# Kernel optimization log

Measured on AMD Instinct MI355X. Metric: run time of the kernel, lower is better.

Reference implementation:

```python
import jax, jax.numpy as jnp
import numpy as np

N = 200000   # nodes
E = 600000   # edges
D = 128      # emb_dim
L = 5        # num_layer
G = 2000     # graphs in batch
T = 1        # num_tasks
NUM_ATOM_TYPE = 120
NUM_CHIRALITY = 3
NUM_BOND_TYPE = 6
NUM_BOND_DIR = 3
EPS = 1e-5


def setup_inputs() -> dict:
    key = jax.random.key(0)
    ks = jax.random.split(key, 16)
    s = lambda k, shape, fan: jax.random.normal(k, shape, jnp.float32) * (1.0 / np.sqrt(fan))
    return {
        "x_idx": jax.random.randint(ks[0], (N, 2), 0, 3),
        "edge_index": jax.random.randint(ks[1], (2, E), 0, N),
        "edge_attr": jax.random.randint(ks[2], (E, 2), 0, 3),
        "batch": jnp.sort(jax.random.randint(ks[3], (N,), 0, G)),
        "atom_emb1": s(ks[4], (NUM_ATOM_TYPE, D), D),
        "atom_emb2": s(ks[5], (NUM_CHIRALITY, D), D),
        "edge_emb1": s(ks[6], (L, NUM_BOND_TYPE, D), D),
        "edge_emb2": s(ks[7], (L, NUM_BOND_DIR, D), D),
        "W1": s(ks[8], (L, D, 2 * D), D),
        "b1": jnp.zeros((L, 2 * D), jnp.float32),
        "W2": s(ks[9], (L, 2 * D, D), 2 * D),
        "b2": jnp.zeros((L, D), jnp.float32),
        "bn_gamma": jnp.ones((L, D), jnp.float32),
        "bn_beta": jnp.zeros((L, D), jnp.float32),
        "Wp": s(ks[10], (D, T), D),
        "bp": jnp.zeros((T,), jnp.float32),
    }


def reference(atom_emb1, atom_emb2, edge_emb1, edge_emb2, W1, b1, W2, b2,
              bn_gamma, bn_beta, Wp, bp, x_idx, edge_index, edge_attr, batch):
    # node input embedding: sum of atom-type and chirality embeddings
    h = atom_emb1[x_idx[:, 0]] + atom_emb2[x_idx[:, 1]]  # [N, D]
    src, dst = edge_index[0], edge_index[1]
    ea0, ea1 = edge_attr[:, 0], edge_attr[:, 1]
    for l in range(L):
        # GINConv: edge embedding + neighbor add-aggregation (incl. self loop, bond type 4 / dir 0)
        e = edge_emb1[l][ea0] + edge_emb2[l][ea1]                 # [E, D]
        msg = h[src] + e                                          # gather + fuse
        agg = jax.ops.segment_sum(msg, dst, num_segments=N)       # scatter-add
        agg = agg + h + (edge_emb1[l][4] + edge_emb2[l][0])       # self-loop message
        # GIN MLP: Linear(D,2D) -> ReLU -> Linear(2D,D)
        z = jnp.maximum(agg @ W1[l] + b1[l], 0.0) @ W2[l] + b2[l]
        # BatchNorm1d over nodes (training-mode batch statistics)
        mu = z.mean(0)
        var = z.var(0)
        z = (z - mu) * jax.lax.rsqrt(var + EPS) * bn_gamma[l] + bn_beta[l]
        # ReLU except after the last layer; dropout ratio is 0 (identity)
        h = jnp.maximum(z, 0.0) if l < L - 1 else z
    # JK 'last' node representation -> sum pooling over graphs -> task head
    pooled = jax.ops.segment_sum(h, batch, num_segments=G)        # [G, D]
    return pooled @ Wp + bp                                       # [G, T]
```

## Files before the change

### kernel.cpp

```cpp
#include <hip/hip_runtime.h>

typedef unsigned int uint;
typedef unsigned short ushort;
typedef _Float16 f16_t;
typedef f16_t f16x8 __attribute__((ext_vector_type(8)));
typedef ushort ushort8 __attribute__((ext_vector_type(8)));
typedef float f32x4 __attribute__((ext_vector_type(4)));

#define NN 200000
#define EE 600000
#define LL 5
#define GG 2000
#define SCAN_NB 782

__device__ __forceinline__ ushort f2h(float f) {
  f16_t h = (f16_t)f;
  return __builtin_bit_cast(ushort, h);
}
__device__ __forceinline__ float h2f(ushort u) {
  return (float)__builtin_bit_cast(f16_t, u);
}
__device__ __forceinline__ float hlo(uint u) { return h2f((ushort)(u & 0xFFFFu)); }
__device__ __forceinline__ float hhi(uint u) { return h2f((ushort)(u >> 16)); }
__device__ __forceinline__ f16x8 ld8h(const uint4* p, int idx) {
  uint4 u = p[idx];
  return __builtin_bit_cast(f16x8, u);
}
__device__ __forceinline__ f16x8 bnrelu8(f16x8 u, f16x8 sc, f16x8 sh) {
  f16x8 r = u * sc + sh;
#pragma unroll
  for (int j = 0; j < 8; ++j) r[j] = r[j] > (f16_t)0.f ? r[j] : (f16_t)0.f;
  return r;
}

__global__ void k_setup(const float* __restrict__ W1, const float* __restrict__ W2,
                        ushort* __restrict__ w1s, ushort* __restrict__ w2s,
                        const float* __restrict__ ee1, const float* __restrict__ ee2,
                        const float* __restrict__ at1, const float* __restrict__ at2,
                        ushort* __restrict__ tabh, const int* __restrict__ xidx,
                        int* __restrict__ xcode, float* __restrict__ out,
                        const float* __restrict__ bp) {
  int i = blockIdx.x * 256 + threadIdx.x;
  if (i < 40960) {
    int lane = i & 63;
    int f = i >> 6;
    bool isW2 = false;
    if (f >= 320) { f -= 320; isW2 = true; }
    int l = f >> 6, rem = f & 63;
    ushort8 o;
    if (!isW2) {
      int kt = rem >> 4, nt = rem & 15;
      int n = nt * 16 + (lane & 15);
      int kbase = kt * 32 + (lane >> 4) * 8;
#pragma unroll
      for (int j = 0; j < 8; ++j) o[j] = f2h(W1[l * 32768 + (kbase + j) * 256 + n]);
      *(ushort8*)(w1s + f * 512 + lane * 8) = o;
    } else {
      int kt = rem >> 3, nt = rem & 7;
      int n = nt * 16 + (lane & 15);
      int kbase = kt * 32 + (lane >> 4) * 8;
#pragma unroll
      for (int j = 0; j < 8; ++j) o[j] = f2h(W2[l * 32768 + (kbase + j) * 128 + n]);
      *(ushort8*)(w2s + f * 512 + lane * 8) = o;
    }
  }
  if (i < 5760) {
    int l = i / 1152, rem = i % 1152;
    int ab = rem >> 7, c = rem & 127;
    int a = ab / 3, b = ab - a * 3;
    tabh[i] = f2h(ee1[(l * 6 + a) * 128 + c] + ee2[(l * 3 + b) * 128 + c]);
  } else if (i < 6400) {
    int j = i - 5760;
    int l = j >> 7, c = j & 127;
    tabh[i] = f2h(ee1[(l * 6 + 4) * 128 + c] + ee2[(l * 3 + 0) * 128 + c]);
  } else if (i < 7552) {
    int j = i - 6400;
    int ab = j >> 7, c = j & 127;
    int a = ab / 3, b = ab - a * 3;
    tabh[i] = f2h(at1[a * 128 + c] + at2[b * 128 + c]);
  }
  if (i < NN) xcode[i] = xidx[2 * i] * 3 + xidx[2 * i + 1];
  if (i < GG) out[i] = bp[0];
}

__global__ void k_count(const int* __restrict__ ei, int* __restrict__ counts) {
  int e = blockIdx.x * 256 + threadIdx.x;
  if (e < EE) atomicAdd(&counts[ei[EE + e]], 1);
}

__global__ void k_scanA(const int* __restrict__ counts, int* __restrict__ rowptr,
                        int* __restrict__ bsums) {
  __shared__ int sd[256];
  int tid = threadIdx.x;
  int g = blockIdx.x * 256 + tid;
  int v = (g < NN) ? counts[g] : 0;
  sd[tid] = v;
  __syncthreads();
  for (int o = 1; o < 256; o <<= 1) {
    int t = (tid >= o) ? sd[tid - o] : 0;
    __syncthreads();
    sd[tid] += t;
    __syncthreads();
  }
  if (g < NN) rowptr[g] = sd[tid] - v;
  if (tid == 255) bsums[blockIdx.x] = sd[tid];
}

__global__ void k_scanB(int* __restrict__ bsums) {
  __shared__ int sd[1024];
  int tid = threadIdx.x;
  int v = (tid < SCAN_NB) ? bsums[tid] : 0;
  sd[tid] = v;
  __syncthreads();
  for (int o = 1; o < 1024; o <<= 1) {
    int t = (tid >= o) ? sd[tid - o] : 0;
    __syncthreads();
    sd[tid] += t;
    __syncthreads();
  }
  if (tid < SCAN_NB) bsums[tid] = sd[tid] - v;
}

__global__ void k_scanC(int* __restrict__ rowptr, const int* __restrict__ bsums) {
  int g = blockIdx.x * 256 + threadIdx.x;
  if (g < NN) rowptr[g] += bsums[blockIdx.x];
  if (g == 0) rowptr[NN] = EE;
}

__global__ void k_fill(const int* __restrict__ ei, const int* __restrict__ ea,
                       const int* __restrict__ xcode, int* __restrict__ cursor,
                       int* __restrict__ eslot) {
  int e = blockIdx.x * 256 + threadIdx.x;
  if (e < EE) {
    int dst = ei[EE + e];
    int src = ei[e];
    int a9 = ea[2 * e] * 3 + ea[2 * e + 1];
    int sc = xcode[src];
    int pos = atomicAdd(&cursor[dst], 1);
    eslot[pos] = src | (a9 << 18) | (sc << 22);
  }
}

__global__ void k_hist2(const int* __restrict__ rowptr, int* __restrict__ bhist) {
  __shared__ int h[256];
  int tid = threadIdx.x;
  h[tid] = 0;
  __syncthreads();
  int n = blockIdx.x * 256 + tid;
  if (n < NN) {
    int d = rowptr[n + 1] - rowptr[n];
    if (d > 255) d = 255;
    atomicAdd(&h[d], 1);
  }
  __syncthreads();
  bhist[tid * SCAN_NB + blockIdx.x] = h[tid];
}

__global__ void k_hscanA(int* __restrict__ data, int* __restrict__ bsums) {
  __shared__ int sd[256];
  int tid = threadIdx.x;
  int g = blockIdx.x * 256 + tid;
  int v = data[g];
  sd[tid] = v;
  __syncthreads();
  for (int o = 1; o < 256; o <<= 1) {
    int t = (tid >= o) ? sd[tid - o] : 0;
    __syncthreads();
    sd[tid] += t;
    __syncthreads();
  }
  data[g] = sd[tid] - v;
  if (tid == 255) bsums[blockIdx.x] = sd[tid];
}

__global__ void k_hscanC(int* __restrict__ data, const int* __restrict__ bsums) {
  int g = blockIdx.x * 256 + threadIdx.x;
  data[g] += bsums[blockIdx.x];
}

__global__ void k_dfill2(const int* __restrict__ rowptr, const int* __restrict__ xcode,
                         const int* __restrict__ bpos, int4* __restrict__ ndesc) {
  __shared__ int h[256];
  int tid = threadIdx.x;
  h[tid] = 0;
  __syncthreads();
  int n = blockIdx.x * 256 + tid;
  if (n < NN) {
    int s = rowptr[n], e = rowptr[n + 1];
    int d = e - s;
    if (d > 255) d = 255;
    int r = atomicAdd(&h[d], 1);
    int pos = bpos[d * SCAN_NB + blockIdx.x] + r;
    ndesc[pos] = make_int4(n, s, e, xcode[n]);
  }
}

__global__ __launch_bounds__(256, 5) void k_layer(
    const ushort* __restrict__ zin, ushort* __restrict__ zout,
    const int4* __restrict__ ndesc, const ushort* __restrict__ tabh,
    const float* __restrict__ bnscale, const float* __restrict__ bnshift,
    const int* __restrict__ eslot,
    const ushort* __restrict__ w1s, const ushort* __restrict__ w2s,
    const float* __restrict__ b1, const float* __restrict__ b2,
    float* __restrict__ stats, int layer) {
  __shared__ __align__(16) ushort BUF[32 * 264];
  __shared__ int4 ND[32];
  ushort* AGG = BUF;
  ushort* T1 = BUF;
  ushort* ldsZ = BUF;
  const int tid = threadIdx.x;
  const int w = tid >> 6, lane = tid & 63;
  const int ln16 = lane & 15, sub = lane >> 4;
  const int row0 = blockIdx.x * 32;

  if (tid < 32) ND[tid] = ndesc[row0 + tid];
  __syncthreads();

  const uint4* combH = (const uint4*)(tabh + (size_t)layer * 1152);
  const uint4* atomH = (const uint4*)(tabh + 6400);
  const uint4* selfH = (const uint4*)(tabh + 5760 + layer * 128);
  const uint4* h4 = (const uint4*)zin;
  f16x8 sf = ld8h(selfH, ln16);
  f16x8 scv = {}, shv = {};
  if (layer > 0) {
    const float* sp = bnscale + (layer - 1) * 128 + ln16 * 8;
    const float* hp = bnshift + (layer - 1) * 128 + ln16 * 8;
#pragma unroll
    for (int j = 0; j < 8; ++j) {
      scv[j] = (f16_t)sp[j];
      shv[j] = (f16_t)hp[j];
    }
  }

#pragma unroll
  for (int grp = 0; grp < 2; ++grp) {
    const int4 nd = ND[w * 8 + grp * 4 + sub];
    const int n = nd.x;
    const int s = nd.y, e = nd.z;
    f16x8 acc;
    if (layer == 0) {
      acc = ld8h(atomH, nd.w * 16 + ln16) + sf;
    } else {
      acc = bnrelu8(ld8h(h4, (size_t)n * 16 + ln16), scv, shv) + sf;
    }
    for (int base = s; base < e; base += 16) {
      int m = e - base;
      if (m > 16) m = 16;
      int slot = (ln16 < m) ? eslot[base + ln16] : 0;
      int jfull = m & ~3;
      int j = 0;
      for (; j < jfull; j += 4) {
        int sl0 = __shfl(slot, sub * 16 + j + 0, 64);
        int sl1 = __shfl(slot, sub * 16 + j + 1, 64);
        int sl2 = __shfl(slot, sub * 16 + j + 2, 64);
        int sl3 = __shfl(slot, sub * 16 + j + 3, 64);
        f16x8 p0, p1, p2, p3;
        if (layer == 0) {
          p0 = ld8h(atomH, ((sl0 >> 22) & 15) * 16 + ln16);
          p1 = ld8h(atomH, ((sl1 >> 22) & 15) * 16 + ln16);
          p2 = ld8h(atomH, ((sl2 >> 22) & 15) * 16 + ln16);
          p3 = ld8h(atomH, ((sl3 >> 22) & 15) * 16 + ln16);
        } else {
          p0 = ld8h(h4, (size_t)(sl0 & 0x3FFFF) * 16 + ln16);
          p1 = ld8h(h4, (size_t)(sl1 & 0x3FFFF) * 16 + ln16);
          p2 = ld8h(h4, (size_t)(sl2 & 0x3FFFF) * 16 + ln16);
          p3 = ld8h(h4, (size_t)(sl3 & 0x3FFFF) * 16 + ln16);
        }
        f16x8 c0 = ld8h(combH, ((sl0 >> 18) & 15) * 16 + ln16);
        f16x8 c1 = ld8h(combH, ((sl1 >> 18) & 15) * 16 + ln16);
        f16x8 c2 = ld8h(combH, ((sl2 >> 18) & 15) * 16 + ln16);
        f16x8 c3 = ld8h(combH, ((sl3 >> 18) & 15) * 16 + ln16);
        if (layer != 0) {
          p0 = bnrelu8(p0, scv, shv);
          p1 = bnrelu8(p1, scv, shv);
          p2 = bnrelu8(p2, scv, shv);
          p3 = bnrelu8(p3, scv, shv);
        }
        acc += p0 + c0;
        acc += p1 + c1;
        acc += p2 + c2;
        acc += p3 + c3;
      }
      for (; j < m; ++j) {
        int sl = __shfl(slot, sub * 16 + j, 64);
        f16x8 p0;
        if (layer == 0) {
          p0 = ld8h(atomH, ((sl >> 22) & 15) * 16 + ln16);
        } else {
          p0 = bnrelu8(ld8h(h4, (size_t)(sl & 0x3FFFF) * 16 + ln16), scv, shv);
        }
        f16x8 c0 = ld8h(combH, ((sl >> 18) & 15) * 16 + ln16);
        acc += p0 + c0;
      }
    }
    *(uint4*)&AGG[(w * 8 + grp * 4 + sub) * 136 + ln16 * 8] =
        __builtin_bit_cast(uint4, acc);
  }
  __syncthreads();

  const int lm = ln16, q = sub;
  f32x4 acc[2][4] = {};
  const ushort* w1b = w1s + layer * 64 * 512;
#pragma unroll
  for (int kt = 0; kt < 4; ++kt) {
    f16x8 af[2];
#pragma unroll
    for (int mt = 0; mt < 2; ++mt) {
      const ushort* p = AGG + (mt * 16 + lm) * 136 + kt * 32 + q * 8;
      af[mt] = __builtin_bit_cast(f16x8, *(const ushort8*)p);
    }
#pragma unroll
    for (int np = 0; np < 2; ++np) {
      f16x8 bf[2];
#pragma unroll
      for (int ni = 0; ni < 2; ++ni) {
        const ushort* p = w1b + (kt * 16 + w * 4 + np * 2 + ni) * 512 + lane * 8;
        bf[ni] = __builtin_bit_cast(f16x8, *(const ushort8*)p);
      }
#pragma unroll
      for (int mt = 0; mt < 2; ++mt)
#pragma unroll
        for (int ni = 0; ni < 2; ++ni)
          acc[mt][np * 2 + ni] = __builtin_amdgcn_mfma_f32_16x16x32_f16(
              af[mt], bf[ni], acc[mt][np * 2 + ni], 0, 0, 0);
    }
  }
  __syncthreads();
#pragma unroll
  for (int nt = 0; nt < 4; ++nt) {
    int n = w * 64 + nt * 16 + lm;
    float bias = b1[layer * 256 + n];
#pragma unroll
    for (int mt = 0; mt < 2; ++mt)
#pragma unroll
      for (int r = 0; r < 4; ++r) {
        float v = fmaxf(acc[mt][nt][r] + bias, 0.0f);
        T1[(mt * 16 + q * 4 + r) * 264 + n] = f2h(v);
      }
  }
  __syncthreads();

  f32x4 acc2[2][2] = {};
  const ushort* w2b = w2s + layer * 64 * 512;
#pragma unroll
  for (int kt = 0; kt < 8; ++kt) {
    f16x8 af[2], bf[2];
#pragma unroll
    for (int mt = 0; mt < 2; ++mt) {
      const ushort* p = T1 + (mt * 16 + lm) * 264 + kt * 32 + q * 8;
      af[mt] = __builtin_bit_cast(f16x8, *(const ushort8*)p);
    }
#pragma unroll
    for (int nt = 0; nt < 2; ++nt) {
      const ushort* p = w2b + (kt * 8 + w * 2 + nt) * 512 + lane * 8;
      bf[nt] = __builtin_bit_cast(f16x8, *(const ushort8*)p);
    }
#pragma unroll
    for (int mt = 0; mt < 2; ++mt)
#pragma unroll
      for (int nt = 0; nt < 2; ++nt)
        acc2[mt][nt] = __builtin_amdgcn_mfma_f32_16x16x32_f16(af[mt], bf[nt], acc2[mt][nt], 0, 0, 0);
  }
  __syncthreads();
  float ssum[2], ssq[2];
#pragma unroll
  for (int nt = 0; nt < 2; ++nt) {
    int n = w * 32 + nt * 16 + lm;
    float bias = b2[layer * 128 + n];
    ssum[nt] = 0.f;
    ssq[nt] = 0.f;
#pragma unroll
    for (int mt = 0; mt < 2; ++mt)
#pragma unroll
      for (int r = 0; r < 4; ++r) {
        float v = acc2[mt][nt][r] + bias;
        ldsZ[(mt * 16 + q * 4 + r) * 136 + n] = f2h(v);
        ssum[nt] += v;
        ssq[nt] += v * v;
      }
    ssum[nt] += __shfl_xor(ssum[nt], 16, 64);
    ssum[nt] += __shfl_xor(ssum[nt], 32, 64);
    ssq[nt] += __shfl_xor(ssq[nt], 16, 64);
    ssq[nt] += __shfl_xor(ssq[nt], 32, 64);
  }
  if (lane < 16) {
    int cp = blockIdx.x & 15;
    float* sb = stats + (size_t)(layer * 16 + cp) * 256;
#pragma unroll
    for (int nt = 0; nt < 2; ++nt) {
      int col = w * 32 + nt * 16 + lane;
      atomicAdd(&sb[col], ssum[nt]);
      atomicAdd(&sb[128 + col], ssq[nt]);
    }
  }
  __syncthreads();
  uint* zo = (uint*)zout;
  for (int i = tid; i < 32 * 64; i += 256) {
    int row = i >> 6, cpx = i & 63;
    uint v = *(const uint*)&ldsZ[row * 136 + cpx * 2];
    zo[(size_t)ND[row].x * 64 + cpx] = v;
  }
}

__global__ void k_bnparam(const float* __restrict__ stats, const float* __restrict__ gamma,
                          const float* __restrict__ beta, float* __restrict__ bnscale,
                          float* __restrict__ bnshift, int layer) {
  int c = threadIdx.x;
  float s = 0.f, qv = 0.f;
  for (int cp = 0; cp < 16; ++cp) {
    const float* sb = stats + (size_t)(layer * 16 + cp) * 256;
    s += sb[c];
    qv += sb[128 + c];
  }
  float mu = s * (1.0f / NN);
  float var = qv * (1.0f / NN) - mu * mu;
  float sc = gamma[layer * 128 + c] * rsqrtf(var + 1e-5f);
  bnscale[layer * 128 + c] = sc;
  bnshift[layer * 128 + c] = beta[layer * 128 + c] - mu * sc;
}

__global__ __launch_bounds__(256) void k_pool(const ushort* __restrict__ z,
                                              const float* __restrict__ bnscale,
                                              const float* __restrict__ bnshift,
                                              const int* __restrict__ batch,
                                              const float* __restrict__ Wp,
                                              float* __restrict__ out) {
  const int tid = threadIdx.x;
  const int w = tid >> 6, lane = tid & 63;
  const int nb = blockIdx.x * 64 + w * 16;
  float2 wp = ((const float2*)Wp)[lane];
  float2 scv = ((const float2*)(bnscale + 4 * 128))[lane];
  float2 shv = ((const float2*)(bnshift + 4 * 128))[lane];
  const uint* z32 = (const uint*)z;
  int bb = (lane < 16) ? batch[nb + lane] : 0;
  int curb = __shfl(bb, 0);
  float run = 0.f;
#pragma unroll
  for (int i = 0; i < 16; ++i) {
    int b = __shfl(bb, i);
    uint u = z32[(size_t)(nb + i) * 64 + lane];
    float dot = fmaf(hlo(u), scv.x, shv.x) * wp.x + fmaf(hhi(u), scv.y, shv.y) * wp.y;
#pragma unroll
    for (int off = 32; off > 0; off >>= 1) dot += __shfl_xor(dot, off, 64);
    if (b != curb) {
      if (lane == 0) atomicAdd(&out[curb], run);
      run = 0.f;
      curb = b;
    }
    run += dot;
  }
  if (lane == 0) atomicAdd(&out[curb], run);
}

extern "C" void kernel_launch(void* const* d_in, const int* in_sizes, int n_in,
                              void* d_out, int out_size, void* d_ws, size_t ws_size,
                              hipStream_t stream) {
  (void)in_sizes; (void)n_in; (void)out_size; (void)ws_size;
  const int* xidx = (const int*)d_in[0];
  const int* eidx = (const int*)d_in[1];
  const int* eattr = (const int*)d_in[2];
  const int* batch = (const int*)d_in[3];
  const float* at1 = (const float*)d_in[4];
  const float* at2 = (const float*)d_in[5];
  const float* ee1 = (const float*)d_in[6];
  const float* ee2 = (const float*)d_in[7];
  const float* W1 = (const float*)d_in[8];
  const float* b1 = (const float*)d_in[9];
  const float* W2 = (const float*)d_in[10];
  const float* b2 = (const float*)d_in[11];
  const float* gamma = (const float*)d_in[12];
  const float* beta = (const float*)d_in[13];
  const float* Wp = (const float*)d_in[14];
  const float* bp = (const float*)d_in[15];
  float* out = (float*)d_out;

  char* ws = (char*)d_ws;
  size_t off = 0;
  auto alloc = [&](size_t bytes) -> void* {
    void* p = ws + off;
    off = (off + bytes + 255) & ~(size_t)255;
    return p;
  };
  ushort* bufA = (ushort*)alloc((size_t)NN * 128 * 2);
  ushort* bufB = (ushort*)alloc((size_t)NN * 128 * 2);
  ushort* w1s = (ushort*)alloc(320 * 512 * 2);
  ushort* w2s = (ushort*)alloc(320 * 512 * 2);
  int* rowptr = (int*)alloc((NN + 1) * 4);
  int* cursor = (int*)alloc((size_t)NN * 4);
  int* eslot = (int*)alloc((size_t)EE * 4);
  int* bsums = (int*)alloc(1024 * 4);
  ushort* tabh = (ushort*)alloc(7552 * 2);
  int* xcode = (int*)alloc((size_t)NN * 4);
  float* stats = (float*)alloc((size_t)LL * 16 * 256 * 4);
  float* bnscale = (float*)alloc(LL * 128 * 4);
  float* bnshift = (float*)alloc(LL * 128 * 4);
  int* bhist = (int*)alloc((size_t)SCAN_NB * 256 * 4);
  int* bsums2 = (int*)alloc(1024 * 4);
  int4* ndesc = (int4*)alloc((size_t)NN * 16);

  hipMemsetAsync(cursor, 0, (size_t)NN * 4, stream);
  hipMemsetAsync(stats, 0, (size_t)LL * 16 * 256 * 4, stream);
  k_setup<<<SCAN_NB, 256, 0, stream>>>(W1, W2, w1s, w2s, ee1, ee2, at1, at2, tabh, xidx,
                                       xcode, out, bp);
  k_count<<<(EE + 255) / 256, 256, 0, stream>>>(eidx, cursor);
  k_scanA<<<SCAN_NB, 256, 0, stream>>>(cursor, rowptr, bsums);
  k_scanB<<<1, 1024, 0, stream>>>(bsums);
  k_scanC<<<SCAN_NB, 256, 0, stream>>>(rowptr, bsums);
  hipMemcpyAsync(cursor, rowptr, (size_t)NN * 4, hipMemcpyDeviceToDevice, stream);
  k_fill<<<(EE + 255) / 256, 256, 0, stream>>>(eidx, eattr, xcode, cursor, eslot);
  k_hist2<<<SCAN_NB, 256, 0, stream>>>(rowptr, bhist);
  k_hscanA<<<SCAN_NB, 256, 0, stream>>>(bhist, bsums2);
  k_scanB<<<1, 1024, 0, stream>>>(bsums2);
  k_hscanC<<<SCAN_NB, 256, 0, stream>>>(bhist, bsums2);
  k_dfill2<<<SCAN_NB, 256, 0, stream>>>(rowptr, xcode, bhist, ndesc);

  for (int l = 0; l < LL; ++l) {
    ushort* zo = (l & 1) ? bufB : bufA;
    const ushort* zi = (l & 1) ? bufA : bufB;
    k_layer<<<NN / 32, 256, 0, stream>>>((l == 0) ? bufA : zi, zo, ndesc, tabh, bnscale,
                                         bnshift, eslot, w1s, w2s, b1, b2,
                                         stats, l);
    k_bnparam<<<1, 128, 0, stream>>>(stats, gamma, beta, bnscale, bnshift, l);
  }
  k_pool<<<NN / 64, 256, 0, stream>>>(bufA, bnscale, bnshift, batch, Wp, out);
}
```

Baseline: 555.3 us.

## Fold BN parameter computation into layer and pool kernels; reverse degree ordering

Removes the separate single-block k_bnparam launch after each layer. Every k_layer and k_pool block now reduces the 16 partial stat slices and computes the BN scale and shift into shared memory itself. It also reverses the degree bucketing so nodes are processed highest-degree first, which should improve load balance at the tail. In exchange, each block redundantly reads 16x256 stats floats and pays an extra barrier.

```diff
diff --git a/kernel.cpp b/kernel.cpp
--- a/kernel.cpp
+++ b/kernel.cpp
@@ -150,7 +150,7 @@
   if (n < NN) {
     int d = rowptr[n + 1] - rowptr[n];
     if (d > 255) d = 255;
-    atomicAdd(&h[d], 1);
+    atomicAdd(&h[255 - d], 1);
   }
   __syncthreads();
   bhist[tid * SCAN_NB + blockIdx.x] = h[tid];
@@ -189,8 +189,8 @@
     int s = rowptr[n], e = rowptr[n + 1];
     int d = e - s;
     if (d > 255) d = 255;
-    int r = atomicAdd(&h[d], 1);
-    int pos = bpos[d * SCAN_NB + blockIdx.x] + r;
+    int r = atomicAdd(&h[255 - d], 1);
+    int pos = bpos[(255 - d) * SCAN_NB + blockIdx.x] + r;
     ndesc[pos] = make_int4(n, s, e, xcode[n]);
   }
 }
@@ -198,13 +198,16 @@
 __global__ __launch_bounds__(256, 5) void k_layer(
     const ushort* __restrict__ zin, ushort* __restrict__ zout,
     const int4* __restrict__ ndesc, const ushort* __restrict__ tabh,
-    const float* __restrict__ bnscale, const float* __restrict__ bnshift,
+    const float* __restrict__ stats_in, const float* __restrict__ gamma,
+    const float* __restrict__ beta,
     const int* __restrict__ eslot,
     const ushort* __restrict__ w1s, const ushort* __restrict__ w2s,
     const float* __restrict__ b1, const float* __restrict__ b2,
     float* __restrict__ stats, int layer) {
   __shared__ __align__(16) ushort BUF[32 * 264];
   __shared__ int4 ND[32];
+  __shared__ float SS[256];
+  __shared__ float BNP[256];
   ushort* AGG = BUF;
   ushort* T1 = BUF;
   ushort* ldsZ = BUF;
@@ -214,6 +217,21 @@
   const int row0 = blockIdx.x * 32;
 
   if (tid < 32) ND[tid] = ndesc[row0 + tid];
+  if (layer > 0) {
+    const float* sb = stats_in + (size_t)(layer - 1) * 16 * 256;
+    float a = 0.f;
+#pragma unroll
+    for (int cp = 0; cp < 16; ++cp) a += sb[cp * 256 + tid];
+    SS[tid] = a;
+    __syncthreads();
+    if (tid < 128) {
+      float mu = SS[tid] * (1.0f / NN);
+      float var = SS[128 + tid] * (1.0f / NN) - mu * mu;
+      float sc = gamma[(layer - 1) * 128 + tid] * rsqrtf(var + 1e-5f);
+      BNP[tid] = sc;
+      BNP[128 + tid] = beta[(layer - 1) * 128 + tid] - mu * sc;
+    }
+  }
   __syncthreads();
 
   const uint4* combH = (const uint4*)(tabh + (size_t)layer * 1152);
@@ -223,12 +241,10 @@
   f16x8 sf = ld8h(selfH, ln16);
   f16x8 scv = {}, shv = {};
   if (layer > 0) {
-    const float* sp = bnscale + (layer - 1) * 128 + ln16 * 8;
-    const float* hp = bnshift + (layer - 1) * 128 + ln16 * 8;
 #pragma unroll
     for (int j = 0; j < 8; ++j) {
-      scv[j] = (f16_t)sp[j];
-      shv[j] = (f16_t)hp[j];
+      scv[j] = (f16_t)BNP[ln16 * 8 + j];
+      shv[j] = (f16_t)BNP[128 + ln16 * 8 + j];
     }
   }
 
@@ -402,35 +418,37 @@
   }
 }
 
-__global__ void k_bnparam(const float* __restrict__ stats, const float* __restrict__ gamma,
-                          const float* __restrict__ beta, float* __restrict__ bnscale,
-                          float* __restrict__ bnshift, int layer) {
-  int c = threadIdx.x;
-  float s = 0.f, qv = 0.f;
-  for (int cp = 0; cp < 16; ++cp) {
-    const float* sb = stats + (size_t)(layer * 16 + cp) * 256;
-    s += sb[c];
-    qv += sb[128 + c];
-  }
-  float mu = s * (1.0f / NN);
-  float var = qv * (1.0f / NN) - mu * mu;
-  float sc = gamma[layer * 128 + c] * rsqrtf(var + 1e-5f);
-  bnscale[layer * 128 + c] = sc;
-  bnshift[layer * 128 + c] = beta[layer * 128 + c] - mu * sc;
-}
-
 __global__ __launch_bounds__(256) void k_pool(const ushort* __restrict__ z,
-                                              const float* __restrict__ bnscale,
-                                              const float* __restrict__ bnshift,
+                                              const float* __restrict__ stats,
+                                              const float* __restrict__ gamma,
+                                              const float* __restrict__ beta,
                                               const int* __restrict__ batch,
                                               const float* __restrict__ Wp,
                                               float* __restrict__ out) {
+  __shared__ float SS[256];
+  __shared__ float BNP[256];
   const int tid = threadIdx.x;
   const int w = tid >> 6, lane = tid & 63;
   const int nb = blockIdx.x * 64 + w * 16;
+  {
+    const float* sb = stats + (size_t)4 * 16 * 256;
+    float a = 0.f;
+#pragma unroll
+    for (int cp = 0; cp < 16; ++cp) a += sb[cp * 256 + tid];
+    SS[tid] = a;
+    __syncthreads();
+    if (tid < 128) {
+      float mu = SS[tid] * (1.0f / NN);
+      float var = SS[128 + tid] * (1.0f / NN) - mu * mu;
+      float sc = gamma[4 * 128 + tid] * rsqrtf(var + 1e-5f);
+      BNP[tid] = sc;
+      BNP[128 + tid] = beta[4 * 128 + tid] - mu * sc;
+    }
+    __syncthreads();
+  }
   float2 wp = ((const float2*)Wp)[lane];
-  float2 scv = ((const float2*)(bnscale + 4 * 128))[lane];
-  float2 shv = ((const float2*)(bnshift + 4 * 128))[lane];
+  float2 scv = make_float2(BNP[2 * lane], BNP[2 * lane + 1]);
+  float2 shv = make_float2(BNP[128 + 2 * lane], BNP[128 + 2 * lane + 1]);
   const uint* z32 = (const uint*)z;
   int bb = (lane < 16) ? batch[nb + lane] : 0;
   int curb = __shfl(bb, 0);
@@ -492,8 +510,6 @@
   ushort* tabh = (ushort*)alloc(7552 * 2);
   int* xcode = (int*)alloc((size_t)NN * 4);
   float* stats = (float*)alloc((size_t)LL * 16 * 256 * 4);
-  float* bnscale = (float*)alloc(LL * 128 * 4);
-  float* bnshift = (float*)alloc(LL * 128 * 4);
   int* bhist = (int*)alloc((size_t)SCAN_NB * 256 * 4);
   int* bsums2 = (int*)alloc(1024 * 4);
   int4* ndesc = (int4*)alloc((size_t)NN * 16);
@@ -517,10 +533,9 @@
   for (int l = 0; l < LL; ++l) {
     ushort* zo = (l & 1) ? bufB : bufA;
     const ushort* zi = (l & 1) ? bufA : bufB;
-    k_layer<<<NN / 32, 256, 0, stream>>>((l == 0) ? bufA : zi, zo, ndesc, tabh, bnscale,
-                                         bnshift, eslot, w1s, w2s, b1, b2,
+    k_layer<<<NN / 32, 256, 0, stream>>>((l == 0) ? bufA : zi, zo, ndesc, tabh, stats,
+                                         gamma, beta, eslot, w1s, w2s, b1, b2,
                                          stats, l);
-    k_bnparam<<<1, 128, 0, stream>>>(stats, gamma, beta, bnscale, bnshift, l);
-  }
-  k_pool<<<NN / 64, 256, 0, stream>>>(bufA, bnscale, bnshift, batch, Wp, out);
-}
+  }
+  k_pool<<<NN / 64, 256, 0, stream>>>(bufA, stats, gamma, beta, batch, Wp, out);
+}
```

After: 553.7 us. Within noise of the previous version (-0.3%).
